# Kernel optimization log

Measured on AMD Instinct MI355X. Metric: run time of the kernel, lower is better.

## Reference

```python
import jax, jax.numpy as jnp
import numpy as np

BETA = 0.25  # commitment loss weight (beta)
EPS_NORM = 1e-12  # F.normalize eps


def l2norm(t):
    return t / jnp.clip(jnp.linalg.norm(t, axis=-1, keepdims=True), EPS_NORM)


def setup_inputs() -> dict:
    key = jax.random.key(0)
    k1, k2 = jax.random.split(key)
    z = jax.random.normal(k1, (16, 256, 32, 32), dtype=jnp.float32)
    # EmbeddingEMA with kmeans_init=False: weight = l2norm(randn(n_embed, dim))
    weight = l2norm(jax.random.normal(k2, (8192, 256), dtype=jnp.float32))
    return {"z": z, "weight": weight}


def reference(z, weight):
    # z: [B, C, H, W] -> [B, H, W, C], l2-normalized per token
    zc = l2norm(jnp.transpose(z, (0, 2, 3, 1)))
    B, H, W, D = zc.shape
    zf = zc.reshape(-1, D)  # [N, D]
    zf_d = jax.lax.stop_gradient(zf)
    # negative squared L2 distance: -|z|^2 - |w|^2 + 2 z.w  -> argmax = nearest code
    d = (-jnp.sum(zf_d ** 2, axis=1, keepdims=True)
         - jnp.sum(weight ** 2, axis=1)
         + 2.0 * jnp.einsum('nd,kd->nk', zf_d, weight))  # [N, K]
    idx = jnp.argmax(d, axis=1)  # [N]
    z_q = weight[idx].reshape(B, H, W, D)  # codebook gather
    # commitment loss: beta * mean((sg(z_q) - z)^2)
    loss = BETA * jnp.mean((jax.lax.stop_gradient(z_q) - zc) ** 2)
    # straight-through estimator
    z_q = zc + jax.lax.stop_gradient(z_q - zc)
    z_q = jnp.transpose(z_q, (0, 3, 1, 2))  # back to [B, C, H, W]
    return z_q, loss, idx
```

## Files before the change

kernel.cpp:

```cpp
#include <hip/hip_runtime.h>
#include <math.h>

#define BB   16
#define CC   256
#define HW   1024
#define NN   16384
#define DD   256
#define KK   8192
#define ZQ_SIZE 4194304
#define MARGIN 0.017f
#define GCAP 8192

typedef __attribute__((ext_vector_type(8))) short short8;
typedef __attribute__((ext_vector_type(4))) float f32x4;

static __device__ inline unsigned short f2bf(float x) {
    unsigned int u = __float_as_uint(x);
    unsigned int r = (u + 0x7fff + ((u >> 16) & 1)) >> 16;
    return (unsigned short)r;
}

static __device__ inline unsigned long long pack_key(float s, int k) {
    unsigned int bits = __float_as_uint(s);
    unsigned int o = (bits & 0x80000000u) ? ~bits : (bits | 0x80000000u);
    return ((unsigned long long)o << 32) | (unsigned int)(~k);
}

__global__ __launch_bounds__(256) void wsq_kernel(const float* __restrict__ W,
                                                  float* __restrict__ wsq,
                                                  int* __restrict__ gcnt,
                                                  int* __restrict__ oflow) {
    if (blockIdx.x == 0) {
        gcnt[threadIdx.x] = 0;
        if (threadIdx.x == 0) *oflow = 0;
    }
    const int lane = threadIdx.x & 63;
    const int k = blockIdx.x * 4 + (threadIdx.x >> 6);
    float4 v = *(const float4*)(W + (size_t)k * DD + lane * 4);
    float s = v.x * v.x + v.y * v.y + v.z * v.z + v.w * v.w;
    #pragma unroll
    for (int off = 32; off; off >>= 1) s += __shfl_down(s, off);
    if (lane == 0) wsq[k] = s;
}

__global__ __launch_bounds__(256) void normalize_kernel(const float* __restrict__ z,
                                                        float* __restrict__ zn,
                                                        float* __restrict__ znsq,
                                                        unsigned short* __restrict__ zb) {
    __shared__ float tile[64][257];
    __shared__ float s_nrm[64];
    const int t   = threadIdx.x;
    const int b   = blockIdx.x >> 4;
    const int hw0 = (blockIdx.x & 15) * 64;

    #pragma unroll 8
    for (int cg = 0; cg < 64; ++cg) {
        int c  = cg * 4 + (t >> 6);
        int hw = t & 63;
        tile[hw][c] = z[((size_t)(b * CC + c) << 10) + hw0 + hw];
    }
    __syncthreads();
    if (t < 64) {
        float s = 0.f;
        #pragma unroll 8
        for (int c = 0; c < 256; ++c) { float v = tile[t][c]; s += v * v; }
        float nrm = sqrtf(s);
        nrm = fmaxf(nrm, 1e-12f);
        s_nrm[t] = nrm;
        znsq[(size_t)b * HW + hw0 + t] = s / (nrm * nrm);
    }
    __syncthreads();
    const int n0 = b * HW + hw0;
    for (int r = 0; r < 64; ++r) {
        zn[(size_t)(n0 + r) * DD + t] = tile[r][t] / s_nrm[r];
    }
    const int r    = t & 63;
    const int mt   = n0 >> 7;
    const int rg   = (n0 & 127) + r;
    const float nrm = s_nrm[r];
    #pragma unroll
    for (int loop = 0; loop < 8; ++loop) {
        int comb = loop * 4 + (t >> 6);
        int dc = comb >> 3, c = comb & 7;
        int d0 = dc * 64 + c * 8;
        uint4 out;
        out.x = (unsigned int)f2bf(tile[r][d0 + 0] / nrm) | ((unsigned int)f2bf(tile[r][d0 + 1] / nrm) << 16);
        out.y = (unsigned int)f2bf(tile[r][d0 + 2] / nrm) | ((unsigned int)f2bf(tile[r][d0 + 3] / nrm) << 16);
        out.z = (unsigned int)f2bf(tile[r][d0 + 4] / nrm) | ((unsigned int)f2bf(tile[r][d0 + 5] / nrm) << 16);
        out.w = (unsigned int)f2bf(tile[r][d0 + 6] / nrm) | ((unsigned int)f2bf(tile[r][d0 + 7] / nrm) << 16);
        *(uint4*)(zb + (size_t)(mt * 4 + dc) * 8192 + (size_t)(c * 128 + rg) * 8) = out;
    }
}

__global__ __launch_bounds__(256) void wb_convert_kernel(const float* __restrict__ W,
                                                         unsigned short* __restrict__ wb) {
    const int ch = blockIdx.x * 256 + threadIdx.x;
    const int c = (ch >> 7) & 7;
    const int r = ch & 127;
    const int kt = ch >> 12, dc = (ch >> 10) & 3;
    const int k = kt * 128 + r;
    const int d0 = dc * 64 + c * 8;
    const float4 v0 = *(const float4*)(W + (size_t)k * DD + d0);
    const float4 v1 = *(const float4*)(W + (size_t)k * DD + d0 + 4);
    uint4 out;
    out.x = (unsigned int)f2bf(v0.x) | ((unsigned int)f2bf(v0.y) << 16);
    out.y = (unsigned int)f2bf(v0.z) | ((unsigned int)f2bf(v0.w) << 16);
    out.z = (unsigned int)f2bf(v1.x) | ((unsigned int)f2bf(v1.y) << 16);
    out.w = (unsigned int)f2bf(v1.z) | ((unsigned int)f2bf(v1.w) << 16);
    *(uint4*)(wb + (size_t)ch * 8) = out;
}

__global__ __launch_bounds__(256) void score_kernel(const unsigned short* __restrict__ zb,
                                                    const unsigned short* __restrict__ wb,
                                                    const float* __restrict__ wsqv,
                                                    float* __restrict__ cmax) {
    __shared__ unsigned short sA[8192];
    __shared__ unsigned short sB[8192];
    __shared__ float rowbuf[128][4];

    const int tid  = threadIdx.x;
    const int w    = tid >> 6;
    const int lane = tid & 63;
    const int wr   = w >> 1, wc = w & 1;
    const int q    = lane >> 4, c15 = lane & 15;
    const int kt   = blockIdx.x & 63;
    const int mt   = blockIdx.x >> 6;

    f32x4 acc[4][4];
    #pragma unroll
    for (int fi = 0; fi < 4; ++fi)
        #pragma unroll
        for (int fj = 0; fj < 4; ++fj)
            acc[fi][fj] = (f32x4){0.f, 0.f, 0.f, 0.f};

    for (int dc = 0; dc < 4; ++dc) {
        const unsigned short* gA = zb + (size_t)(mt * 4 + dc) * 8192;
        const unsigned short* gB = wb + (size_t)(kt * 4 + dc) * 8192;
        #pragma unroll
        for (int i = 0; i < 4; ++i) {
            int eo = ((w * 4 + i) << 9);
            __builtin_amdgcn_global_load_lds(
                (const __attribute__((address_space(1))) void*)(gA + eo + lane * 8),
                (__attribute__((address_space(3))) void*)(sA + eo), 16, 0, 0);
            __builtin_amdgcn_global_load_lds(
                (const __attribute__((address_space(1))) void*)(gB + eo + lane * 8),
                (__attribute__((address_space(3))) void*)(sB + eo), 16, 0, 0);
        }
        __syncthreads();
        #pragma unroll
        for (int ks = 0; ks < 2; ++ks) {
            short8 af[4], bfr[4];
            const int ca = (ks * 4 + q) * 128;
            #pragma unroll
            for (int f = 0; f < 4; ++f) {
                af[f]  = *(const short8*)(sA + (size_t)(ca + wr * 64 + f * 16 + c15) * 8);
                bfr[f] = *(const short8*)(sB + (size_t)(ca + wc * 64 + f * 16 + c15) * 8);
            }
            #pragma unroll
            for (int fi = 0; fi < 4; ++fi)
                #pragma unroll
                for (int fj = 0; fj < 4; ++fj)
                    acc[fi][fj] = __builtin_amdgcn_mfma_f32_16x16x32_bf16(
                        af[fi], bfr[fj], acc[fi][fj], 0, 0, 0);
        }
        __syncthreads();
    }

    float wsqc[4];
    #pragma unroll
    for (int fj = 0; fj < 4; ++fj)
        wsqc[fj] = wsqv[kt * 128 + wc * 64 + fj * 16 + c15];

    #pragma unroll
    for (int fi = 0; fi < 4; ++fi) {
        float vmx[2][4];
        #pragma unroll
        for (int fjp = 0; fjp < 2; ++fjp) {
            #pragma unroll
            for (int rg = 0; rg < 4; ++rg) {
                float a0 = 2.0f * acc[fi][2 * fjp][rg]     - wsqc[2 * fjp];
                float a1 = 2.0f * acc[fi][2 * fjp + 1][rg] - wsqc[2 * fjp + 1];
                float v = fmaxf(a0, a1);
                v = fmaxf(v, __shfl_xor(v, 1));
                v = fmaxf(v, __shfl_xor(v, 2));
                v = fmaxf(v, __shfl_xor(v, 4));
                v = fmaxf(v, __shfl_xor(v, 8));
                vmx[fjp][rg] = v;
            }
        }
        if (c15 < 4) {
            int row = wr * 64 + fi * 16 + q * 4 + c15;
            rowbuf[row][wc * 2 + 0] = vmx[0][c15];
            rowbuf[row][wc * 2 + 1] = vmx[1][c15];
        }
    }
    __syncthreads();
    {
        int row = tid >> 1, half = tid & 1;
        float2 v2 = make_float2(rowbuf[row][half * 2], rowbuf[row][half * 2 + 1]);
        *(float2*)(cmax + (size_t)(mt * 128 + row) * 256 + kt * 4 + half * 2) = v2;
    }
}

__global__ __launch_bounds__(256) void cand_kernel(const float* __restrict__ cmax,
                                                   unsigned int* __restrict__ gseg,
                                                   int* __restrict__ gcnt,
                                                   unsigned long long* __restrict__ packed,
                                                   int* __restrict__ nflag,
                                                   int* __restrict__ oflow) {
    const int t = threadIdx.x, wv = t >> 6, lane = t & 63;
    const int n = blockIdx.x * 4 + wv;
    float4 c4 = *(const float4*)(cmax + (size_t)n * 256 + lane * 4);
    float lm = fmaxf(fmaxf(c4.x, c4.y), fmaxf(c4.z, c4.w));
    #pragma unroll
    for (int off = 1; off <= 32; off <<= 1) lm = fmaxf(lm, __shfl_xor(lm, off));
    const float thresh = lm - MARGIN;
    if (lane == 0) { packed[n] = 0ull; nflag[n] = 0; }
    float g4[4] = {c4.x, c4.y, c4.z, c4.w};
    #pragma unroll
    for (int j = 0; j < 4; ++j) {
        int g = lane * 4 + j;
        if (g4[j] >= thresh) {
            int pos = atomicAdd(&gcnt[g], 1);
            if (pos < GCAP) gseg[(size_t)g * GCAP + pos] = (unsigned int)n;
            else { nflag[n] = 1; atomicAdd(oflow, 1); }
        }
    }
}

__global__ __launch_bounds__(256) void rescore_kernel(const float* __restrict__ zn,
                                                      const float* __restrict__ W,
                                                      const float* __restrict__ wsqv,
                                                      const float* __restrict__ znsq,
                                                      const unsigned int* __restrict__ gseg,
                                                      const int* __restrict__ gcnt,
                                                      unsigned long long* __restrict__ packed) {
    __shared__ float sW[32 * 260];
    __shared__ float znr[4][2][256];

    const int t = threadIdx.x;
    const int g = blockIdx.x;
    int cnt = gcnt[g]; if (cnt > GCAP) cnt = GCAP;
    if (cnt == 0) return;

    {
        int c = t >> 3, i = t & 7;
        const float4* src = (const float4*)(W + (size_t)g * 8192 + c * 256 + i * 32);
        #pragma unroll
        for (int j = 0; j < 8; ++j)
            *(float4*)(sW + c * 260 + i * 32 + j * 4) = src[j];
    }
    __syncthreads();

    const int wv = t >> 6, lane = t & 63;
    const int h = lane >> 5, c = lane & 31;
    const int k = g * 32 + c;
    const float wq = wsqv[k];
    const float4* wrow = (const float4*)(sW + c * 260);

    for (int base = wv * 2; base < cnt; base += 8) {
        int idx = base + h; if (idx >= cnt) idx = base;
        int n = (int)gseg[(size_t)g * GCAP + idx];
        *(float4*)(&znr[wv][h][c * 8])     = *(const float4*)(zn + (size_t)n * DD + c * 8);
        *(float4*)(&znr[wv][h][c * 8 + 4]) = *(const float4*)(zn + (size_t)n * DD + c * 8 + 4);
        float d = 0.f;
        #pragma unroll
        for (int j = 0; j < 64; ++j) {
            float4 wv4 = wrow[j];
            float4 zv  = *(const float4*)(&znr[wv][h][j * 4]);
            d += wv4.x * zv.x + wv4.y * zv.y + wv4.z * zv.z + wv4.w * zv.w;
        }
        float s = (-znsq[n] - wq) + 2.0f * d;
        unsigned long long key = pack_key(s, k);
        #pragma unroll
        for (int off = 1; off <= 16; off <<= 1) {
            unsigned long long ok = __shfl_xor(key, off);
            if (ok > key) key = ok;
        }
        if (c == 0) atomicMax(packed + n, key);
    }
}

__global__ __launch_bounds__(256) void fullscan_kernel(const float* __restrict__ zn,
                                                       const float* __restrict__ W,
                                                       const float* __restrict__ wsqv,
                                                       const float* __restrict__ znsq,
                                                       const int* __restrict__ nflag,
                                                       const int* __restrict__ oflow,
                                                       unsigned long long* __restrict__ packed) {
    if (*oflow == 0) return;
    const int t = threadIdx.x, wv = t >> 6, lane = t & 63;
    const int code = lane >> 1, part = lane & 1;
    for (int n = blockIdx.x * 4 + wv; n < NN; n += gridDim.x * 4) {
        if (!nflag[n]) continue;
        float zsq = znsq[n];
        unsigned long long best = 0ull;
        for (int gg = 0; gg < 256; ++gg) {
            int k = gg * 32 + code;
            const float4* wrp = (const float4*)(W + (size_t)k * DD + part * 128);
            const float4* zrp = (const float4*)(zn + (size_t)n * DD + part * 128);
            float d = 0.f;
            #pragma unroll
            for (int jj = 0; jj < 32; ++jj) {
                float4 a = zrp[jj], b = wrp[jj];
                d += a.x * b.x + a.y * b.y + a.z * b.z + a.w * b.w;
            }
            d += __shfl_xor(d, 1);
            unsigned long long key = pack_key((-zsq - wsqv[k]) + 2.0f * d, k);
            if (key > best) best = key;
        }
        #pragma unroll
        for (int off = 1; off <= 32; off <<= 1) {
            unsigned long long ok = __shfl_xor(best, off);
            if (ok > best) best = ok;
        }
        if (lane == 0) atomicMax(packed + n, best);
    }
}

__global__ __launch_bounds__(256) void gatherfin_kernel(const float* __restrict__ W,
                                                        const unsigned long long* __restrict__ packed,
                                                        float* __restrict__ idxf,
                                                        float* __restrict__ partials,
                                                        float* __restrict__ zq) {
    __shared__ int sbk[64];
    const int t   = threadIdx.x;
    const int b   = blockIdx.x >> 4;
    const int hw0 = (blockIdx.x & 15) * 64;
    if (t < 64) {
        int n = b * HW + hw0 + t;
        unsigned long long key = packed[n];
        int k = (int)((~(unsigned int)key) & 0x3FFFu);
        unsigned int o = (unsigned int)(key >> 32);
        unsigned int bits = (o & 0x80000000u) ? (o & 0x7FFFFFFFu) : ~o;
        float s = __uint_as_float(bits);
        sbk[t] = k;
        idxf[n] = (float)k;
        float cc = -s;
        #pragma unroll
        for (int off = 32; off; off >>= 1) cc += __shfl_down(cc, off);
        if (t == 0) partials[blockIdx.x] = cc;
    }
    __syncthreads();
    const int hw  = t & 63;
    const int c0  = (t >> 6) * 4;
    const int row = sbk[hw];
    #pragma unroll
    for (int cg = 0; cg < 16; ++cg) {
        int c = cg * 16 + c0;
        float4 v = *(const float4*)(W + (size_t)row * DD + c);
        size_t base = ((size_t)(b * CC + c) << 10) + hw0 + hw;
        zq[base]        = v.x;
        zq[base + 1024] = v.y;
        zq[base + 2048] = v.z;
        zq[base + 3072] = v.w;
    }
}

__global__ __launch_bounds__(256) void loss_final_kernel(const float* __restrict__ partials,
                                                         float* __restrict__ out_loss) {
    __shared__ float wsum[4];
    const int t = threadIdx.x;
    float v = partials[t];
    #pragma unroll
    for (int off = 32; off; off >>= 1) v += __shfl_down(v, off);
    if ((t & 63) == 0) wsum[t >> 6] = v;
    __syncthreads();
    if (t == 0) {
        float tot = wsum[0] + wsum[1] + wsum[2] + wsum[3];
        *out_loss = 0.25f * (tot / (float)ZQ_SIZE);
    }
}

extern "C" void kernel_launch(void* const* d_in, const int* in_sizes, int n_in,
                              void* d_out, int out_size, void* d_ws, size_t ws_size,
                              hipStream_t stream) {
    const float* z = (const float*)d_in[0];
    const float* W = (const float*)d_in[1];

    float* out   = (float*)d_out;
    float* zq    = out;
    float* loss  = out + ZQ_SIZE;
    float* idxf  = out + ZQ_SIZE + 1;

    float* ws       = (float*)d_ws;
    float* zn       = ws;
    float* znsq     = zn + (size_t)NN * DD;
    float* wsqv     = znsq + NN;
    float* partials = wsqv + KK;
    int*   gcnt     = (int*)(partials + 256);
    int*   oflow    = gcnt + 256;
    int*   nflag    = oflow + 64;
    unsigned short* zb = (unsigned short*)(nflag + NN);
    unsigned short* wb = zb + (size_t)NN * DD;
    float* cmax     = (float*)(wb + (size_t)KK * DD);
    unsigned int* gseg = (unsigned int*)(cmax + (size_t)NN * 256);
    unsigned long long* packed = (unsigned long long*)(gseg + (size_t)256 * GCAP);

    wsq_kernel       <<<KK / 4, 256, 0, stream>>>(W, wsqv, gcnt, oflow);
    normalize_kernel <<<BB * 16, 256, 0, stream>>>(z, zn, znsq, zb);
    wb_convert_kernel<<<KK * DD / 8 / 256, 256, 0, stream>>>(W, wb);
    score_kernel     <<<(NN / 128) * (KK / 128), 256, 0, stream>>>(zb, wb, wsqv, cmax);
    cand_kernel      <<<NN / 4, 256, 0, stream>>>(cmax, gseg, gcnt, packed, nflag, oflow);
    rescore_kernel   <<<256, 256, 0, stream>>>(zn, W, wsqv, znsq, gseg, gcnt, packed);
    fullscan_kernel  <<<64, 256, 0, stream>>>(zn, W, wsqv, znsq, nflag, oflow, packed);
    gatherfin_kernel <<<BB * 16, 256, 0, stream>>>(W, packed, idxf, partials, zq);
    loss_final_kernel<<<1, 256, 0, stream>>>(partials, loss);
}
```

Measured before the change: 290.2 us.

## Split rescore across more blocks, fuse wb conversion, vectorize normalize loads, swap score roles

Rescore work per codebook group is split across eight blocks, so 2048 blocks launch instead of 256, raising parallelism in the candidate rescoring stage. The bf16 codebook conversion is folded into the wsq kernel to remove one launch. Normalize now reads z with float4 loads. The score kernel swaps the MFMA operand roles so the row-max reduction needs fewer cross-lane shuffles, and it stages wsq in shared memory. Each rescore block still loads its full 32-row W slice into shared memory, so that load is repeated eight times per group.

```diff
diff --git a/kernel.cpp b/kernel.cpp
--- a/kernel.cpp
+++ b/kernel.cpp
@@ -10,6 +10,7 @@
 #define ZQ_SIZE 4194304
 #define MARGIN 0.017f
 #define GCAP 8192
+#define RSPLIT 8
 
 typedef __attribute__((ext_vector_type(8))) short short8;
 typedef __attribute__((ext_vector_type(4))) float f32x4;
@@ -26,21 +27,40 @@
     return ((unsigned long long)o << 32) | (unsigned int)(~k);
 }
 
-__global__ __launch_bounds__(256) void wsq_kernel(const float* __restrict__ W,
-                                                  float* __restrict__ wsq,
-                                                  int* __restrict__ gcnt,
-                                                  int* __restrict__ oflow) {
+__global__ __launch_bounds__(256) void wsqwb_kernel(const float* __restrict__ W,
+                                                    float* __restrict__ wsq,
+                                                    unsigned short* __restrict__ wb,
+                                                    int* __restrict__ gcnt,
+                                                    int* __restrict__ oflow) {
     if (blockIdx.x == 0) {
         gcnt[threadIdx.x] = 0;
         if (threadIdx.x == 0) *oflow = 0;
     }
-    const int lane = threadIdx.x & 63;
-    const int k = blockIdx.x * 4 + (threadIdx.x >> 6);
-    float4 v = *(const float4*)(W + (size_t)k * DD + lane * 4);
-    float s = v.x * v.x + v.y * v.y + v.z * v.z + v.w * v.w;
-    #pragma unroll
-    for (int off = 32; off; off >>= 1) s += __shfl_down(s, off);
-    if (lane == 0) wsq[k] = s;
+    {
+        const int lane = threadIdx.x & 63;
+        const int k = blockIdx.x * 4 + (threadIdx.x >> 6);
+        float4 v = *(const float4*)(W + (size_t)k * DD + lane * 4);
+        float s = v.x * v.x + v.y * v.y + v.z * v.z + v.w * v.w;
+        #pragma unroll
+        for (int off = 32; off; off >>= 1) s += __shfl_down(s, off);
+        if (lane == 0) wsq[k] = s;
+    }
+    if (blockIdx.x < 1024) {
+        const int ch = blockIdx.x * 256 + threadIdx.x;
+        const int c = (ch >> 7) & 7;
+        const int r = ch & 127;
+        const int kt = ch >> 12, dc = (ch >> 10) & 3;
+        const int k = kt * 128 + r;
+        const int d0 = dc * 64 + c * 8;
+        const float4 v0 = *(const float4*)(W + (size_t)k * DD + d0);
+        const float4 v1 = *(const float4*)(W + (size_t)k * DD + d0 + 4);
+        uint4 out;
+        out.x = (unsigned int)f2bf(v0.x) | ((unsigned int)f2bf(v0.y) << 16);
+        out.y = (unsigned int)f2bf(v0.z) | ((unsigned int)f2bf(v0.w) << 16);
+        out.z = (unsigned int)f2bf(v1.x) | ((unsigned int)f2bf(v1.y) << 16);
+        out.w = (unsigned int)f2bf(v1.z) | ((unsigned int)f2bf(v1.w) << 16);
+        *(uint4*)(wb + (size_t)ch * 8) = out;
+    }
 }
 
 __global__ __launch_bounds__(256) void normalize_kernel(const float* __restrict__ z,
@@ -53,11 +73,15 @@
     const int b   = blockIdx.x >> 4;
     const int hw0 = (blockIdx.x & 15) * 64;
 
-    #pragma unroll 8
-    for (int cg = 0; cg < 64; ++cg) {
-        int c  = cg * 4 + (t >> 6);
-        int hw = t & 63;
-        tile[hw][c] = z[((size_t)(b * CC + c) << 10) + hw0 + hw];
+    #pragma unroll
+    for (int cg = 0; cg < 16; ++cg) {
+        int c  = cg * 16 + (t >> 4);
+        int hw = (t & 15) * 4;
+        float4 v = *(const float4*)(z + ((size_t)(b * CC + c) << 10) + hw0 + hw);
+        tile[hw + 0][c] = v.x;
+        tile[hw + 1][c] = v.y;
+        tile[hw + 2][c] = v.z;
+        tile[hw + 3][c] = v.w;
     }
     __syncthreads();
     if (t < 64) {
@@ -92,24 +116,6 @@
     }
 }
 
-__global__ __launch_bounds__(256) void wb_convert_kernel(const float* __restrict__ W,
-                                                         unsigned short* __restrict__ wb) {
-    const int ch = blockIdx.x * 256 + threadIdx.x;
-    const int c = (ch >> 7) & 7;
-    const int r = ch & 127;
-    const int kt = ch >> 12, dc = (ch >> 10) & 3;
-    const int k = kt * 128 + r;
-    const int d0 = dc * 64 + c * 8;
-    const float4 v0 = *(const float4*)(W + (size_t)k * DD + d0);
-    const float4 v1 = *(const float4*)(W + (size_t)k * DD + d0 + 4);
-    uint4 out;
-    out.x = (unsigned int)f2bf(v0.x) | ((unsigned int)f2bf(v0.y) << 16);
-    out.y = (unsigned int)f2bf(v0.z) | ((unsigned int)f2bf(v0.w) << 16);
-    out.z = (unsigned int)f2bf(v1.x) | ((unsigned int)f2bf(v1.y) << 16);
-    out.w = (unsigned int)f2bf(v1.z) | ((unsigned int)f2bf(v1.w) << 16);
-    *(uint4*)(wb + (size_t)ch * 8) = out;
-}
-
 __global__ __launch_bounds__(256) void score_kernel(const unsigned short* __restrict__ zb,
                                                     const unsigned short* __restrict__ wb,
                                                     const float* __restrict__ wsqv,
@@ -117,14 +123,18 @@
     __shared__ unsigned short sA[8192];
     __shared__ unsigned short sB[8192];
     __shared__ float rowbuf[128][4];
+    __shared__ __align__(16) float swsq[128];
 
     const int tid  = threadIdx.x;
     const int w    = tid >> 6;
     const int lane = tid & 63;
-    const int wr   = w >> 1, wc = w & 1;
+    const int wcr  = w >> 1;
+    const int wct  = w & 1;
     const int q    = lane >> 4, c15 = lane & 15;
     const int kt   = blockIdx.x & 63;
     const int mt   = blockIdx.x >> 6;
+
+    if (tid < 128) swsq[tid] = wsqv[kt * 128 + tid];
 
     f32x4 acc[4][4];
     #pragma unroll
@@ -149,49 +159,49 @@
         __syncthreads();
         #pragma unroll
         for (int ks = 0; ks < 2; ++ks) {
-            short8 af[4], bfr[4];
+            short8 tfr[4], cfr[4];
             const int ca = (ks * 4 + q) * 128;
             #pragma unroll
             for (int f = 0; f < 4; ++f) {
-                af[f]  = *(const short8*)(sA + (size_t)(ca + wr * 64 + f * 16 + c15) * 8);
-                bfr[f] = *(const short8*)(sB + (size_t)(ca + wc * 64 + f * 16 + c15) * 8);
+                tfr[f] = *(const short8*)(sA + (size_t)(ca + wct * 64 + f * 16 + c15) * 8);
+                cfr[f] = *(const short8*)(sB + (size_t)(ca + wcr * 64 + f * 16 + c15) * 8);
             }
             #pragma unroll
             for (int fi = 0; fi < 4; ++fi)
                 #pragma unroll
                 for (int fj = 0; fj < 4; ++fj)
                     acc[fi][fj] = __builtin_amdgcn_mfma_f32_16x16x32_bf16(
-                        af[fi], bfr[fj], acc[fi][fj], 0, 0, 0);
+                        cfr[fi], tfr[fj], acc[fi][fj], 0, 0, 0);
         }
         __syncthreads();
     }
 
-    float wsqc[4];
-    #pragma unroll
-    for (int fj = 0; fj < 4; ++fj)
-        wsqc[fj] = wsqv[kt * 128 + wc * 64 + fj * 16 + c15];
-
-    #pragma unroll
-    for (int fi = 0; fi < 4; ++fi) {
-        float vmx[2][4];
-        #pragma unroll
-        for (int fjp = 0; fjp < 2; ++fjp) {
+    f32x4 wq4[4];
+    #pragma unroll
+    for (int fi = 0; fi < 4; ++fi)
+        wq4[fi] = *(const f32x4*)(&swsq[wcr * 64 + fi * 16 + q * 4]);
+
+    #pragma unroll
+    for (int fj = 0; fj < 4; ++fj) {
+        float g[2];
+        #pragma unroll
+        for (int p = 0; p < 2; ++p) {
+            float vm = -INFINITY;
             #pragma unroll
-            for (int rg = 0; rg < 4; ++rg) {
-                float a0 = 2.0f * acc[fi][2 * fjp][rg]     - wsqc[2 * fjp];
-                float a1 = 2.0f * acc[fi][2 * fjp + 1][rg] - wsqc[2 * fjp + 1];
-                float v = fmaxf(a0, a1);
-                v = fmaxf(v, __shfl_xor(v, 1));
-                v = fmaxf(v, __shfl_xor(v, 2));
-                v = fmaxf(v, __shfl_xor(v, 4));
-                v = fmaxf(v, __shfl_xor(v, 8));
-                vmx[fjp][rg] = v;
+            for (int f2 = 0; f2 < 2; ++f2) {
+                int fi = p * 2 + f2;
+                #pragma unroll
+                for (int rg = 0; rg < 4; ++rg)
+                    vm = fmaxf(vm, 2.0f * acc[fi][fj][rg] - wq4[fi][rg]);
             }
-        }
-        if (c15 < 4) {
-            int row = wr * 64 + fi * 16 + q * 4 + c15;
-            rowbuf[row][wc * 2 + 0] = vmx[0][c15];
-            rowbuf[row][wc * 2 + 1] = vmx[1][c15];
+            vm = fmaxf(vm, __shfl_xor(vm, 16));
+            vm = fmaxf(vm, __shfl_xor(vm, 32));
+            g[p] = vm;
+        }
+        if (q == 0) {
+            int row = wct * 64 + fj * 16 + c15;
+            rowbuf[row][wcr * 2 + 0] = g[0];
+            rowbuf[row][wcr * 2 + 1] = g[1];
         }
     }
     __syncthreads();
@@ -239,9 +249,10 @@
     __shared__ float znr[4][2][256];
 
     const int t = threadIdx.x;
-    const int g = blockIdx.x;
+    const int g   = blockIdx.x >> 3;
+    const int sub = blockIdx.x & 7;
     int cnt = gcnt[g]; if (cnt > GCAP) cnt = GCAP;
-    if (cnt == 0) return;
+    if (cnt <= sub * 8) return;
 
     {
         int c = t >> 3, i = t & 7;
@@ -258,7 +269,7 @@
     const float wq = wsqv[k];
     const float4* wrow = (const float4*)(sW + c * 260);
 
-    for (int base = wv * 2; base < cnt; base += 8) {
+    for (int base = (sub * 4 + wv) * 2; base < cnt; base += RSPLIT * 8) {
         int idx = base + h; if (idx >= cnt) idx = base;
         int n = (int)gseg[(size_t)g * GCAP + idx];
         *(float4*)(&znr[wv][h][c * 8])     = *(const float4*)(zn + (size_t)n * DD + c * 8);
@@ -397,12 +408,11 @@
     unsigned int* gseg = (unsigned int*)(cmax + (size_t)NN * 256);
     unsigned long long* packed = (unsigned long long*)(gseg + (size_t)256 * GCAP);
 
-    wsq_kernel       <<<KK / 4, 256, 0, stream>>>(W, wsqv, gcnt, oflow);
+    wsqwb_kernel     <<<KK / 4, 256, 0, stream>>>(W, wsqv, wb, gcnt, oflow);
     normalize_kernel <<<BB * 16, 256, 0, stream>>>(z, zn, znsq, zb);
-    wb_convert_kernel<<<KK * DD / 8 / 256, 256, 0, stream>>>(W, wb);
     score_kernel     <<<(NN / 128) * (KK / 128), 256, 0, stream>>>(zb, wb, wsqv, cmax);
     cand_kernel      <<<NN / 4, 256, 0, stream>>>(cmax, gseg, gcnt, packed, nflag, oflow);
-    rescore_kernel   <<<256, 256, 0, stream>>>(zn, W, wsqv, znsq, gseg, gcnt, packed);
+    rescore_kernel   <<<256 * RSPLIT, 256, 0, stream>>>(zn, W, wsqv, znsq, gseg, gcnt, packed);
     fullscan_kernel  <<<64, 256, 0, stream>>>(zn, W, wsqv, znsq, nflag, oflow, packed);
     gatherfin_kernel <<<BB * 16, 256, 0, stream>>>(W, packed, idxf, partials, zq);
     loss_final_kernel<<<1, 256, 0, stream>>>(partials, loss);
```

New measurement: 234.3 us, median of 2. 1.24x faster.
